# Kernel optimization log

Measured on AMD Instinct MI355X. Metric: run time of the kernel, lower is better.

Reference implementation:

```python
import jax, jax.numpy as jnp
import numpy as np

OUT, IN = 4096, 4096
B, S = 4, 2048


def _quantize(w):
    # replicate torch LinearAffine8bit.__init__ affine quantization
    min_val, max_val = jnp.min(w), jnp.max(w)
    scale = (max_val - min_val) / 255.0
    zp = 255.0 - max_val / scale
    zp = jnp.clip(zp, 0.0, 255.0)
    zp = jnp.round(zp)
    q = jnp.round(jnp.clip(zp + w / scale, 0.0, 255.0)).astype(jnp.int32)
    return q, scale, zp


def setup_inputs() -> dict:
    key = jax.random.key(0)
    kx, kw, kb = jax.random.split(key, 3)
    x = jax.random.normal(kx, (B, S, IN), dtype=jnp.float32)
    w_fp = jax.random.normal(kw, (OUT, IN), dtype=jnp.float32) * 0.02
    bias = jax.random.normal(kb, (OUT,), dtype=jnp.float32) * 0.01
    qweight, scale, zero_point = _quantize(w_fp)
    return {"x": x, "qweight": qweight, "scale": scale,
            "zero_point": zero_point, "bias": bias}


def reference(x, qweight, scale, zero_point, bias):
    # F.linear(x, scale * (qweight - zero_point), bias)
    w = scale * (qweight.astype(x.dtype) - zero_point)  # [OUT, IN] dequant
    return jnp.einsum('bsi,oi->bso', x, w) + bias
```

## Files before the change

### kernel.cpp

```cpp
#include <hip/hip_runtime.h>
#include <hip/hip_bf16.h>
#include <stdint.h>

#define M_DIM 8192
#define N_DIM 4096
#define K_DIM 4096

typedef __attribute__((ext_vector_type(4))) int i32x4;
typedef __attribute__((ext_vector_type(8))) __bf16 bf16x8;
typedef __attribute__((ext_vector_type(4))) float f32x4;
typedef __attribute__((ext_vector_type(8))) unsigned short ushort8;

__device__ __forceinline__ unsigned short f2bf(float f) {
  union { float f; uint32_t u; } v; v.f = f;
  uint32_t u = v.u;
  return (unsigned short)((u + 0x7FFFu + ((u >> 16) & 1u)) >> 16);
}

__device__ __forceinline__ void gload_lds16(const void* g, void* l) {
  __builtin_amdgcn_global_load_lds((const __attribute__((address_space(1))) void*)g,
                                   (__attribute__((address_space(3))) void*)l,
                                   16, 0, 0);
}

#define RAW_BAR() asm volatile("s_barrier" ::: "memory")
#define VMW(n) asm volatile("s_waitcnt vmcnt(" #n ")" ::: "memory")
#define LGKM0()                                        \
  do {                                                 \
    asm volatile("s_waitcnt lgkmcnt(0)" ::: "memory"); \
    __builtin_amdgcn_sched_barrier(0);                 \
  } while (0)
#define SBAR0() __builtin_amdgcn_sched_barrier(0)

__global__ __launch_bounds__(256) void prepx_kernel(
    const float* __restrict__ x, const float* __restrict__ scale,
    const float* __restrict__ zp, char* __restrict__ xq,
    float* __restrict__ rsw, float* __restrict__ corr) {
  const int row = blockIdx.x;
  const int t = threadIdx.x;
  const float4* xr = (const float4*)(x + (size_t)row * K_DIM);
  float4 v[4];
  float mx = 0.f;
  #pragma unroll
  for (int i = 0; i < 4; ++i) {
    v[i] = xr[i * 256 + t];
    mx = fmaxf(mx, fmaxf(fmaxf(fabsf(v[i].x), fabsf(v[i].y)),
                         fmaxf(fabsf(v[i].z), fabsf(v[i].w))));
  }
  __shared__ float redm[4], reds[4];
  #pragma unroll
  for (int off = 32; off; off >>= 1) mx = fmaxf(mx, __shfl_xor(mx, off));
  if ((t & 63) == 0) redm[t >> 6] = mx;
  __syncthreads();
  mx = fmaxf(fmaxf(redm[0], redm[1]), fmaxf(redm[2], redm[3]));
  mx = fmaxf(mx, 1e-20f);
  const float inv = 127.f / mx;
  float sum = 0.f;
  int* xqo = (int*)xq + (size_t)row * (K_DIM / 4);
  #pragma unroll
  for (int i = 0; i < 4; ++i) {
    sum += v[i].x + v[i].y + v[i].z + v[i].w;
    int q0 = (int)rintf(v[i].x * inv), q1 = (int)rintf(v[i].y * inv);
    int q2 = (int)rintf(v[i].z * inv), q3 = (int)rintf(v[i].w * inv);
    xqo[i * 256 + t] = (q0 & 255) | ((q1 & 255) << 8) | ((q2 & 255) << 16) | (q3 << 24);
  }
  #pragma unroll
  for (int off = 32; off; off >>= 1) sum += __shfl_xor(sum, off);
  if ((t & 63) == 0) reds[t >> 6] = sum;
  __syncthreads();
  if (t == 0) {
    const float sw = scale[0], zw = zp[0];
    rsw[row] = (mx / 127.f) * sw;
    corr[row] = sw * (128.f - zw) * (reds[0] + reds[1] + reds[2] + reds[3]);
  }
}

__global__ void prepw_kernel(const int* __restrict__ q, char* __restrict__ wq) {
  const long long n4 = (long long)N_DIM * K_DIM / 4;
  long long i = (long long)blockIdx.x * blockDim.x + threadIdx.x;
  const long long stride = (long long)gridDim.x * blockDim.x;
  int* wo = (int*)wq;
  for (; i < n4; i += stride) {
    const int4 a = ((const int4*)q)[i];
    wo[i] = ((a.x - 128) & 255) | (((a.y - 128) & 255) << 8) |
            (((a.z - 128) & 255) << 16) | ((a.w - 128) << 24);
  }
}

#define NTILE (K_DIM / 64)
#define BUFB 32768

__global__ __launch_bounds__(512, 2) void gemm256_i8_kernel(
    const char* __restrict__ xq, const char* __restrict__ wq,
    const float* __restrict__ rsw, const float* __restrict__ corr,
    const float* __restrict__ bias, float* __restrict__ out) {
  __shared__ char lds[3 * BUFB];

  const int t = threadIdx.x;
  const int lane = t & 63;
  const int wid = t >> 6;
  const int wr = wid >> 2;
  const int wc = wid & 3;
  const int fr = lane & 15, fq = lane >> 4;

  const int bid = blockIdx.x;
  const int swz = ((bid & 7) << 6) | (bid >> 3);
  const int bx = swz & 15;
  const int by = swz >> 4;
  const int brow = by * 256, bcol = bx * 256;

  const int gsrc = (t & 3) ^ ((t >> 3) & 3);
  const char* gAs = xq + (size_t)(brow + (t >> 2)) * K_DIM + gsrc * 16;
  const char* gBs = wq + (size_t)(bcol + (t >> 2)) * K_DIM + gsrc * 16;

  const int gsel16 = (fq ^ ((fr >> 1) & 3)) * 16;
  const int arow = (wr * 128 + fr) * 64;
  const int brow_o = 16384 + (wc * 64 + fr) * 64;

  i32x4 af[8], bfv[2][4];
  i32x4 acc[8][4] = {};

  #define LD_A(b, m) (*(const i32x4*)(lds + (b) * BUFB + arow + (m) * 1024 + gsel16))
  #define LD_B(b, n) (*(const i32x4*)(lds + (b) * BUFB + brow_o + (n) * 1024 + gsel16))

  #define RD_H1(b, p)                                                          \
    { af[0] = LD_A(b, 0); af[1] = LD_A(b, 1); af[2] = LD_A(b, 2);              \
      af[3] = LD_A(b, 3);                                                      \
      bfv[p][0] = LD_B(b, 0); bfv[p][1] = LD_B(b, 1);                          \
      bfv[p][2] = LD_B(b, 2); bfv[p][3] = LD_B(b, 3); }
  #define RD_H2(b)                                                             \
    { af[4] = LD_A(b, 4); af[5] = LD_A(b, 5); af[6] = LD_A(b, 6);              \
      af[7] = LD_A(b, 7); }

  #define STG(isB, h, tile, b)                                                 \
    do {                                                                       \
      char* l_ = lds + (b) * BUFB + (isB) * 16384 + (h) * 8192 + t * 16;       \
      const char* g_ = ((isB) ? gBs : gAs) + (size_t)(h) * 128 * K_DIM +       \
                       (size_t)(tile) * 64;                                    \
      gload_lds16(g_, l_);                                                     \
    } while (0)

  #define MMQ(MS, p)                                                           \
    __builtin_amdgcn_s_setprio(1);                                             \
    _Pragma("unroll")                                                          \
    for (int m = 0; m < 4; ++m) {                                              \
      _Pragma("unroll")                                                        \
      for (int n = 0; n < 4; ++n)                                              \
        acc[MS + m][n] = __builtin_amdgcn_mfma_i32_16x16x64_i8(                \
            af[MS + m], bfv[p][n], acc[MS + m][n], 0, 0, 0);                   \
    }                                                                          \
    __builtin_amdgcn_s_setprio(0);                                             \
    SBAR0();

  #define PH_A(b, p, STGB_, WT_)                                               \
    LGKM0(); RD_H2(b) MMQ(0, p) STGB_; WT_; RAW_BAR();
  #define PH_B(b, p, STGA_, RDN_)                                              \
    LGKM0(); RDN_ MMQ(4, p) STGA_; RAW_BAR();

  #define TILE_FULL(b, BN, B2, p, np, Xp2)                                     \
    PH_A(b, p, { STG(1, 0, Xp2, B2); STG(1, 1, Xp2, B2); }, VMW(2))            \
    PH_B(b, p, { STG(0, 0, Xp2, B2); STG(0, 1, Xp2, B2); }, RD_H1(BN, np))

  STG(1, 0, 0, 0); STG(1, 1, 0, 0); STG(0, 0, 0, 0); STG(0, 1, 0, 0);
  STG(1, 0, 1, 1); STG(1, 1, 1, 1); STG(0, 0, 1, 1); STG(0, 1, 1, 1);
  VMW(4);
  RAW_BAR();
  RD_H1(0, 0)

  for (int jj = 0; jj < 10; ++jj) {
    const int X = 6 * jj;
    TILE_FULL(0, 1, 2, 0, 1, X + 2)
    TILE_FULL(1, 2, 0, 1, 0, X + 3)
    TILE_FULL(2, 0, 1, 0, 1, X + 4)
    TILE_FULL(0, 1, 2, 1, 0, X + 5)
    TILE_FULL(1, 2, 0, 0, 1, X + 6)
    TILE_FULL(2, 0, 1, 1, 0, X + 7)
  }
  TILE_FULL(0, 1, 2, 0, 1, 62)
  TILE_FULL(1, 2, 0, 1, 0, 63)
  PH_A(2, 0, {}, VMW(0))
  PH_B(2, 0, {}, RD_H1(0, 1))
  PH_A(0, 1, {}, {})
  LGKM0();
  MMQ(4, 1)

  #undef LD_A
  #undef LD_B
  #undef RD_H1
  #undef RD_H2
  #undef STG
  #undef MMQ
  #undef PH_A
  #undef PH_B
  #undef TILE_FULL

  float bv[4];
  #pragma unroll
  for (int n = 0; n < 4; ++n) bv[n] = bias[bcol + wc * 64 + n * 16 + fr];
  #pragma unroll
  for (int m = 0; m < 8; ++m) {
    #pragma unroll
    for (int j = 0; j < 4; ++j) {
      const int row = brow + wr * 128 + m * 16 + fq * 4 + j;
      const float rs_ = rsw[row], co_ = corr[row];
      #pragma unroll
      for (int n = 0; n < 4; ++n) {
        const int col = bcol + wc * 64 + n * 16 + fr;
        out[(size_t)row * N_DIM + col] = (float)acc[m][n][j] * rs_ + co_ + bv[n];
      }
    }
  }
}

__global__ __launch_bounds__(256) void gemm_fallback_kernel(
    const float* __restrict__ x, const int* __restrict__ qw,
    const float* __restrict__ scale, const float* __restrict__ zp,
    const float* __restrict__ bias, float* __restrict__ out) {
  __shared__ unsigned short lds_a[128 * 32];
  __shared__ unsigned short lds_b[128 * 32];
  const int t = threadIdx.x;
  const int lane = t & 63;
  const int wid = t >> 6;
  const int wr = wid >> 1, wc = wid & 1;
  const int fr = lane & 15, fq = lane >> 4;
  const int nwg = gridDim.x;
  const int cpx = nwg >> 3;
  const int bid = blockIdx.x;
  const int swz = (bid & 7) * cpx + (bid >> 3);
  const int bx = swz & 31, by = swz >> 5;
  const int brow = by * 128, bcol = bx * 128;
  const int r0 = t >> 2, c8 = (t & 3) * 8;
  f32x4 acc[4][4] = {};
  const float ss = scale[0], zs = zp[0];
  for (int kk = 0; kk < K_DIM; kk += 32) {
    ushort8 ua[2], ub[2];
    #pragma unroll
    for (int i = 0; i < 2; ++i) {
      const float* gp = x + (size_t)(brow + i * 64 + r0) * K_DIM + kk + c8;
      float4 v0 = *(const float4*)gp;
      float4 v1 = *(const float4*)(gp + 4);
      ua[i][0] = f2bf(v0.x); ua[i][1] = f2bf(v0.y); ua[i][2] = f2bf(v0.z); ua[i][3] = f2bf(v0.w);
      ua[i][4] = f2bf(v1.x); ua[i][5] = f2bf(v1.y); ua[i][6] = f2bf(v1.z); ua[i][7] = f2bf(v1.w);
      const int* qp = qw + (size_t)(bcol + i * 64 + r0) * K_DIM + kk + c8;
      int4 q0 = *(const int4*)qp;
      int4 q1 = *(const int4*)(qp + 4);
      ub[i][0] = f2bf(ss * ((float)q0.x - zs)); ub[i][1] = f2bf(ss * ((float)q0.y - zs));
      ub[i][2] = f2bf(ss * ((float)q0.z - zs)); ub[i][3] = f2bf(ss * ((float)q0.w - zs));
      ub[i][4] = f2bf(ss * ((float)q1.x - zs)); ub[i][5] = f2bf(ss * ((float)q1.y - zs));
      ub[i][6] = f2bf(ss * ((float)q1.z - zs)); ub[i][7] = f2bf(ss * ((float)q1.w - zs));
    }
    __syncthreads();
    #pragma unroll
    for (int i = 0; i < 2; ++i) {
      *(ushort8*)(lds_a + ((size_t)i * 256 + t) * 8) = ua[i];
      *(ushort8*)(lds_b + ((size_t)i * 256 + t) * 8) = ub[i];
    }
    __syncthreads();
    bf16x8 af[4], bfr[4];
    #pragma unroll
    for (int m = 0; m < 4; ++m)
      af[m] = *(const bf16x8*)(lds_a + (wr * 64 + m * 16 + fr) * 32 + fq * 8);
    #pragma unroll
    for (int n = 0; n < 4; ++n)
      bfr[n] = *(const bf16x8*)(lds_b + (wc * 64 + n * 16 + fr) * 32 + fq * 8);
    #pragma unroll
    for (int m = 0; m < 4; ++m)
      #pragma unroll
      for (int n = 0; n < 4; ++n)
        acc[m][n] = __builtin_amdgcn_mfma_f32_16x16x32_bf16(af[m], bfr[n], acc[m][n], 0, 0, 0);
  }
  #pragma unroll
  for (int n = 0; n < 4; ++n) {
    const int col = bcol + wc * 64 + n * 16 + fr;
    const float bvv = bias[col];
    #pragma unroll
    for (int m = 0; m < 4; ++m) {
      const int rowb = brow + wr * 64 + m * 16 + fq * 4;
      #pragma unroll
      for (int j = 0; j < 4; ++j)
        out[(size_t)(rowb + j) * N_DIM + col] = acc[m][n][j] + bvv;
    }
  }
}

extern "C" void kernel_launch(void* const* d_in, const int* in_sizes, int n_in,
                              void* d_out, int out_size, void* d_ws, size_t ws_size,
                              hipStream_t stream) {
  const float* x = (const float*)d_in[0];
  const int* qw = (const int*)d_in[1];
  const float* scale = (const float*)d_in[2];
  const float* zp = (const float*)d_in[3];
  const float* bias = (const float*)d_in[4];
  float* out = (float*)d_out;

  const size_t xq_bytes = (size_t)M_DIM * K_DIM;
  const size_t wq_bytes = (size_t)N_DIM * K_DIM;
  const size_t rsw_bytes = (size_t)M_DIM * 4;
  const size_t need = xq_bytes + wq_bytes + 2 * rsw_bytes;

  if (ws_size >= need) {
    char* xq = (char*)d_ws;
    char* wq = (char*)d_ws + xq_bytes;
    float* rsw = (float*)((char*)d_ws + xq_bytes + wq_bytes);
    float* corr = rsw + M_DIM;
    prepx_kernel<<<M_DIM, 256, 0, stream>>>(x, scale, zp, xq, rsw, corr);
    prepw_kernel<<<2048, 256, 0, stream>>>(qw, wq);
    const int grid = (M_DIM / 256) * (N_DIM / 256);
    gemm256_i8_kernel<<<grid, 512, 0, stream>>>(xq, wq, rsw, corr, bias, out);
  } else {
    const int grid = (M_DIM / 128) * (N_DIM / 128);
    gemm_fallback_kernel<<<grid, 256, 0, stream>>>(x, qw, scale, zp, bias, out);
  }
}
```

Measured before the change: 186.2 us.

## Switch int8 GEMM to 256x128 tiles with 4 waves and double buffering

Replaces the 256x256, 8-wave, triple-buffered int8 MFMA GEMM with a 256x128 tile computed by 4 waves, each still owning 128x64 of output. LDS drops to two 24 KB buffers, and the main loop is rescheduled into eight sub-phases that interleave MFMA quarters with LDS fragment reads and global-to-LDS staging. The goal is to cut LDS footprint and per-block synchronization so more blocks fit per CU with a launch grid twice as large. In exchange, reuse of A data per block is halved, so global traffic for x rises, and two buffers give less latency hiding than three.

```diff
diff --git a/kernel.cpp b/kernel.cpp
--- a/kernel.cpp
+++ b/kernel.cpp
@@ -88,26 +88,26 @@
 }
 
 #define NTILE (K_DIM / 64)
-#define BUFB 32768
-
-__global__ __launch_bounds__(512, 2) void gemm256_i8_kernel(
+#define BUFB 24576
+
+__global__ __launch_bounds__(256, 2) void gemm_i8_kernel(
     const char* __restrict__ xq, const char* __restrict__ wq,
     const float* __restrict__ rsw, const float* __restrict__ corr,
     const float* __restrict__ bias, float* __restrict__ out) {
-  __shared__ char lds[3 * BUFB];
+  __shared__ char lds[2 * BUFB];
 
   const int t = threadIdx.x;
   const int lane = t & 63;
   const int wid = t >> 6;
-  const int wr = wid >> 2;
-  const int wc = wid & 3;
+  const int wr = wid >> 1;
+  const int wc = wid & 1;
   const int fr = lane & 15, fq = lane >> 4;
 
   const int bid = blockIdx.x;
-  const int swz = ((bid & 7) << 6) | (bid >> 3);
-  const int bx = swz & 15;
-  const int by = swz >> 4;
-  const int brow = by * 256, bcol = bx * 256;
+  const int swz = ((bid & 7) << 7) | (bid >> 3);
+  const int bx = swz & 31;
+  const int by = swz >> 5;
+  const int brow = by * 256, bcol = bx * 128;
 
   const int gsrc = (t & 3) ^ ((t >> 3) & 3);
   const char* gAs = xq + (size_t)(brow + (t >> 2)) * K_DIM + gsrc * 16;
@@ -117,82 +117,74 @@
   const int arow = (wr * 128 + fr) * 64;
   const int brow_o = 16384 + (wc * 64 + fr) * 64;
 
-  i32x4 af[8], bfv[2][4];
+  i32x4 af[8], bfv[4];
   i32x4 acc[8][4] = {};
 
   #define LD_A(b, m) (*(const i32x4*)(lds + (b) * BUFB + arow + (m) * 1024 + gsel16))
   #define LD_B(b, n) (*(const i32x4*)(lds + (b) * BUFB + brow_o + (n) * 1024 + gsel16))
 
-  #define RD_H1(b, p)                                                          \
+  #define RD_Q1(b)                                                             \
     { af[0] = LD_A(b, 0); af[1] = LD_A(b, 1); af[2] = LD_A(b, 2);              \
-      af[3] = LD_A(b, 3);                                                      \
-      bfv[p][0] = LD_B(b, 0); bfv[p][1] = LD_B(b, 1);                          \
-      bfv[p][2] = LD_B(b, 2); bfv[p][3] = LD_B(b, 3); }
-  #define RD_H2(b)                                                             \
+      af[3] = LD_A(b, 3); bfv[0] = LD_B(b, 0); bfv[1] = LD_B(b, 1); }
+  #define RD_Q2(b) { bfv[2] = LD_B(b, 2); bfv[3] = LD_B(b, 3); }
+  #define RD_Q3(b)                                                             \
     { af[4] = LD_A(b, 4); af[5] = LD_A(b, 5); af[6] = LD_A(b, 6);              \
       af[7] = LD_A(b, 7); }
 
-  #define STG(isB, h, tile, b)                                                 \
-    do {                                                                       \
-      char* l_ = lds + (b) * BUFB + (isB) * 16384 + (h) * 8192 + t * 16;       \
-      const char* g_ = ((isB) ? gBs : gAs) + (size_t)(h) * 128 * K_DIM +       \
-                       (size_t)(tile) * 64;                                    \
-      gload_lds16(g_, l_);                                                     \
-    } while (0)
-
-  #define MMQ(MS, p)                                                           \
+  #define STG_A(tile, k)                                                       \
+    gload_lds16(gAs + (size_t)(k) * 64 * K_DIM + (size_t)(tile) * 64,          \
+                lds + ((tile) & 1) * BUFB + (k) * 4096 + t * 16)
+  #define STG_B(tile, k)                                                       \
+    gload_lds16(gBs + (size_t)(k) * 64 * K_DIM + (size_t)(tile) * 64,          \
+                lds + ((tile) & 1) * BUFB + 16384 + (k) * 4096 + t * 16)
+
+  #define MMQ(MS, NS)                                                          \
     __builtin_amdgcn_s_setprio(1);                                             \
     _Pragma("unroll")                                                          \
     for (int m = 0; m < 4; ++m) {                                              \
       _Pragma("unroll")                                                        \
-      for (int n = 0; n < 4; ++n)                                              \
-        acc[MS + m][n] = __builtin_amdgcn_mfma_i32_16x16x64_i8(                \
-            af[MS + m], bfv[p][n], acc[MS + m][n], 0, 0, 0);                   \
+      for (int n = 0; n < 2; ++n)                                              \
+        acc[MS + m][NS + n] = __builtin_amdgcn_mfma_i32_16x16x64_i8(           \
+            af[MS + m], bfv[NS + n], acc[MS + m][NS + n], 0, 0, 0);            \
     }                                                                          \
     __builtin_amdgcn_s_setprio(0);                                             \
     SBAR0();
 
-  #define PH_A(b, p, STGB_, WT_)                                               \
-    LGKM0(); RD_H2(b) MMQ(0, p) STGB_; WT_; RAW_BAR();
-  #define PH_B(b, p, STGA_, RDN_)                                              \
-    LGKM0(); RDN_ MMQ(4, p) STGA_; RAW_BAR();
-
-  #define TILE_FULL(b, BN, B2, p, np, Xp2)                                     \
-    PH_A(b, p, { STG(1, 0, Xp2, B2); STG(1, 1, Xp2, B2); }, VMW(2))            \
-    PH_B(b, p, { STG(0, 0, Xp2, B2); STG(0, 1, Xp2, B2); }, RD_H1(BN, np))
-
-  STG(1, 0, 0, 0); STG(1, 1, 0, 0); STG(0, 0, 0, 0); STG(0, 1, 0, 0);
-  STG(1, 0, 1, 1); STG(1, 1, 1, 1); STG(0, 0, 1, 1); STG(0, 1, 1, 1);
-  VMW(4);
+  STG_B(0, 0); STG_B(0, 1); STG_A(0, 0); STG_A(0, 1); STG_A(0, 2); STG_A(0, 3);
+  STG_B(1, 0); STG_B(1, 1); STG_A(1, 0); STG_A(1, 1); STG_A(1, 2); STG_A(1, 3);
+  VMW(6);
   RAW_BAR();
-  RD_H1(0, 0)
-
-  for (int jj = 0; jj < 10; ++jj) {
-    const int X = 6 * jj;
-    TILE_FULL(0, 1, 2, 0, 1, X + 2)
-    TILE_FULL(1, 2, 0, 1, 0, X + 3)
-    TILE_FULL(2, 0, 1, 0, 1, X + 4)
-    TILE_FULL(0, 1, 2, 1, 0, X + 5)
-    TILE_FULL(1, 2, 0, 0, 1, X + 6)
-    TILE_FULL(2, 0, 1, 1, 0, X + 7)
-  }
-  TILE_FULL(0, 1, 2, 0, 1, 62)
-  TILE_FULL(1, 2, 0, 1, 0, 63)
-  PH_A(2, 0, {}, VMW(0))
-  PH_B(2, 0, {}, RD_H1(0, 1))
-  PH_A(0, 1, {}, {})
-  LGKM0();
-  MMQ(4, 1)
+  RD_Q1(0)
+
+  for (int i = 0; i < NTILE / 2 - 1; ++i) {
+    const int E = 2 * i + 2, O = 2 * i + 3;
+    LGKM0(); MMQ(0, 0) RD_Q2(0) RAW_BAR();
+    LGKM0(); MMQ(0, 2) RD_Q3(0) RAW_BAR();
+    LGKM0(); MMQ(4, 0) STG_B(E, 0); STG_B(E, 1); VMW(2); RAW_BAR();
+    MMQ(4, 2) STG_A(E, 0); STG_A(E, 1); RD_Q1(1) RAW_BAR();
+    LGKM0(); MMQ(0, 0) STG_A(E, 2); STG_A(E, 3); RD_Q2(1) RAW_BAR();
+    LGKM0(); MMQ(0, 2) RD_Q3(1) RAW_BAR();
+    LGKM0(); MMQ(4, 0) STG_B(O, 0); STG_B(O, 1); VMW(2); RAW_BAR();
+    MMQ(4, 2) STG_A(O, 0); STG_A(O, 1); STG_A(O, 2); STG_A(O, 3);
+    RD_Q1(0) RAW_BAR();
+  }
+  LGKM0(); MMQ(0, 0) RD_Q2(0) RAW_BAR();
+  LGKM0(); MMQ(0, 2) RD_Q3(0) RAW_BAR();
+  LGKM0(); MMQ(4, 0) VMW(0); RAW_BAR();
+  MMQ(4, 2) RD_Q1(1) RAW_BAR();
+  LGKM0(); MMQ(0, 0) RD_Q2(1) RAW_BAR();
+  LGKM0(); MMQ(0, 2) RD_Q3(1) RAW_BAR();
+  LGKM0(); MMQ(4, 0) RAW_BAR();
+  LGKM0(); MMQ(4, 2)
 
   #undef LD_A
   #undef LD_B
-  #undef RD_H1
-  #undef RD_H2
-  #undef STG
+  #undef RD_Q1
+  #undef RD_Q2
+  #undef RD_Q3
+  #undef STG_A
+  #undef STG_B
   #undef MMQ
-  #undef PH_A
-  #undef PH_B
-  #undef TILE_FULL
 
   float bv[4];
   #pragma unroll
@@ -305,8 +297,8 @@
     float* corr = rsw + M_DIM;
     prepx_kernel<<<M_DIM, 256, 0, stream>>>(x, scale, zp, xq, rsw, corr);
     prepw_kernel<<<2048, 256, 0, stream>>>(qw, wq);
-    const int grid = (M_DIM / 256) * (N_DIM / 256);
-    gemm256_i8_kernel<<<grid, 512, 0, stream>>>(xq, wq, rsw, corr, bias, out);
+    const int grid = (M_DIM / 256) * (N_DIM / 128);
+    gemm_i8_kernel<<<grid, 256, 0, stream>>>(xq, wq, rsw, corr, bias, out);
   } else {
     const int grid = (M_DIM / 128) * (N_DIM / 128);
     gemm_fallback_kernel<<<grid, 256, 0, stream>>>(x, qw, scale, zp, bias, out);
```

Measured after the change: 194.0 us. +4.2%, slower.

## Deepen int8 GEMM LDS pipeline from three to four stage buffers

Applied to the files above, without the earlier changes.

Grows the shared-memory ring from three to four 32KB tile buffers and rewrites the prologue, main loop and epilogue so global-to-LDS loads run three tiles ahead instead of two. The vmcnt waits are loosened to match the extra outstanding loads. The aim is to hide more global load latency behind the MFMA work. In exchange the LDS footprint per block grows, which could limit how many blocks fit per CU, and the tail issues a redundant stage of tile 0.

```diff
diff --git a/kernel.cpp b/kernel.cpp
--- a/kernel.cpp
+++ b/kernel.cpp
@@ -94,7 +94,7 @@
     const char* __restrict__ xq, const char* __restrict__ wq,
     const float* __restrict__ rsw, const float* __restrict__ corr,
     const float* __restrict__ bias, float* __restrict__ out) {
-  __shared__ char lds[3 * BUFB];
+  __shared__ char lds[4 * BUFB];
 
   const int t = threadIdx.x;
   const int lane = t & 63;
@@ -152,37 +152,38 @@
     __builtin_amdgcn_s_setprio(0);                                             \
     SBAR0();
 
-  #define PH_A(b, p, STGB_, WT_)                                               \
-    LGKM0(); RD_H2(b) MMQ(0, p) STGB_; WT_; RAW_BAR();
-  #define PH_B(b, p, STGA_, RDN_)                                              \
-    LGKM0(); RDN_ MMQ(4, p) STGA_; RAW_BAR();
-
-  #define TILE_FULL(b, BN, B2, p, np, Xp2)                                     \
-    PH_A(b, p, { STG(1, 0, Xp2, B2); STG(1, 1, Xp2, B2); }, VMW(2))            \
-    PH_B(b, p, { STG(0, 0, Xp2, B2); STG(0, 1, Xp2, B2); }, RD_H1(BN, np))
+  #define PH_A(b, p, Xp3, B3, WT_)                                             \
+    LGKM0(); RD_H2(b) MMQ(0, p)                                                \
+    STG(1, 0, Xp3, B3); STG(1, 1, Xp3, B3); WT_; RAW_BAR();
+  #define PH_B(bN, p, np, Xp3, B3)                                             \
+    LGKM0(); RD_H1(bN, np) MMQ(4, p)                                           \
+    STG(0, 0, Xp3, B3); STG(0, 1, Xp3, B3); RAW_BAR();
+
+  #define TILE_FULL(b, bN, B3, p, np, Xp3)                                     \
+    PH_A(b, p, Xp3, B3, VMW(6))                                                \
+    PH_B(bN, p, np, Xp3, B3)
 
   STG(1, 0, 0, 0); STG(1, 1, 0, 0); STG(0, 0, 0, 0); STG(0, 1, 0, 0);
   STG(1, 0, 1, 1); STG(1, 1, 1, 1); STG(0, 0, 1, 1); STG(0, 1, 1, 1);
-  VMW(4);
+  STG(1, 0, 2, 2); STG(1, 1, 2, 2); STG(0, 0, 2, 2); STG(0, 1, 2, 2);
+  VMW(8);
   RAW_BAR();
   RD_H1(0, 0)
 
-  for (int jj = 0; jj < 10; ++jj) {
-    const int X = 6 * jj;
-    TILE_FULL(0, 1, 2, 0, 1, X + 2)
-    TILE_FULL(1, 2, 0, 1, 0, X + 3)
-    TILE_FULL(2, 0, 1, 0, 1, X + 4)
-    TILE_FULL(0, 1, 2, 1, 0, X + 5)
-    TILE_FULL(1, 2, 0, 0, 1, X + 6)
-    TILE_FULL(2, 0, 1, 1, 0, X + 7)
-  }
-  TILE_FULL(0, 1, 2, 0, 1, 62)
-  TILE_FULL(1, 2, 0, 1, 0, 63)
-  PH_A(2, 0, {}, VMW(0))
-  PH_B(2, 0, {}, RD_H1(0, 1))
-  PH_A(0, 1, {}, {})
-  LGKM0();
-  MMQ(4, 1)
+  for (int jj = 0; jj < 15; ++jj) {
+    const int X0 = 4 * jj;
+    TILE_FULL(0, 1, 3, 0, 1, X0 + 3)
+    TILE_FULL(1, 2, 0, 1, 0, X0 + 4)
+    TILE_FULL(2, 3, 1, 0, 1, X0 + 5)
+    TILE_FULL(3, 0, 2, 1, 0, X0 + 6)
+  }
+  TILE_FULL(0, 1, 3, 0, 1, 63)
+  PH_A(1, 1, 0, 0, VMW(4))
+  PH_B(2, 1, 0, 0, 0)
+  LGKM0(); RD_H2(2) MMQ(0, 0) VMW(0); RAW_BAR();
+  LGKM0(); RD_H1(3, 1) MMQ(4, 0) RAW_BAR();
+  LGKM0(); RD_H2(3) MMQ(0, 1)
+  LGKM0(); MMQ(4, 1)
 
   #undef LD_A
   #undef LD_B
@@ -211,6 +212,7 @@
     }
   }
 }
+
 
 __global__ __launch_bounds__(256) void gemm_fallback_kernel(
     const float* __restrict__ x, const int* __restrict__ qw,
```

Measured after the change: 182.4 us. -2.0%, faster.
